# Performance work log

Hardware: AMD Instinct MI355X
Metric: run time of the kernel (lower is better)

Reference implementation:

```python
import jax, jax.numpy as jnp
import numpy as np

N_NODES = 10000
N_EDGES = 640000
D = 128


def setup_inputs() -> dict:
    key = jax.random.key(0)
    k1, k2, k3, k4 = jax.random.split(key, 4)
    X = jax.random.normal(k1, (N_NODES, D), dtype=jnp.float32)
    Y = jax.random.normal(k2, (N_EDGES, D), dtype=jnp.float32)
    # nn.Linear(in, out, bias=False): weight shape (out, in), y = Y @ W.T
    W = jax.random.normal(k3, (D, D), dtype=jnp.float32) * (1.0 / np.sqrt(D))
    edge_index = jax.random.randint(k4, (N_EDGES, 2), 0, N_NODES, dtype=jnp.int64)
    return {"X": X, "Y": Y, "W": W, "edge_index": edge_index}


def reference(X, Y, W, edge_index):
    # Edge transform: (E, d_in) @ (d_in, d_out) -> (E, d_out)
    Y_prime = jnp.einsum('ei,oi->eo', Y, W)
    # Scatter-add transformed edge features to source nodes
    src = edge_index[:, 0]
    agg = jax.ops.segment_sum(Y_prime, src, num_segments=X.shape[0])  # (N, d_out)
    # Residual + activation
    X_prime = jax.nn.relu(X + agg)
    return (X_prime, Y_prime)
```

## Files before the change

kernel.cpp:

```cpp
#include <hip/hip_runtime.h>

#define N_NODES 10000
#define N_EDGES 640000
#define DD 128
#define GATHER_BLOCKS (N_NODES / 4)
#define GEMM_BLOCKS   (N_EDGES / 128)

typedef __attribute__((ext_vector_type(8))) short short8;
typedef __attribute__((ext_vector_type(8))) float f32x8;
typedef __attribute__((ext_vector_type(4))) float f32x4;
typedef __attribute__((ext_vector_type(2))) float f32x2;

__device__ __forceinline__ unsigned pack_bf2(float lo, float hi) {
  return __builtin_amdgcn_perm(__float_as_uint(hi), __float_as_uint(lo), 0x07060302u);
}

__device__ __forceinline__ void stage_w(const float* __restrict__ W,
                                        short8* lwr) {
  const int tid = threadIdx.x;
#pragma unroll
  for (int t = 0; t < 8; ++t) {
    int s = t * 256 + tid;
    f32x8 v = *(const f32x8*)(W + (size_t)s * 8);
    short8 av;
    unsigned* au = (unsigned*)&av;
    au[0] = pack_bf2(v[0], v[1]);
    au[1] = pack_bf2(v[2], v[3]);
    au[2] = pack_bf2(v[4], v[5]);
    au[3] = pack_bf2(v[6], v[7]);
    int j = s >> 4;
    int c = s & 15;
    lwr[(j << 4) | (c ^ (j & 7))] = av;
  }
  __syncthreads();
}

__global__ __launch_bounds__(256) void k_zero(int* __restrict__ count) {
  const int i = blockIdx.x * 256 + threadIdx.x;
  if (i < N_NODES) count[i] = 0;
}

__global__ __launch_bounds__(256) void k_hist(const int* __restrict__ EI,
                                              int* __restrict__ count) {
  const int e = blockIdx.x * 256 + threadIdx.x;
  atomicAdd(&count[EI[2 * e]], 1);
}

__global__ __launch_bounds__(1024) void k_scan(const int* __restrict__ count,
                                               int* __restrict__ rowptr,
                                               int* __restrict__ cursor) {
  __shared__ int part[1024];
  const int tid = threadIdx.x;
  const int base = tid * 10;
  int local[10];
  int s = 0;
#pragma unroll
  for (int i = 0; i < 10; ++i) {
    const int idx = base + i;
    const int v = (idx < N_NODES) ? count[idx] : 0;
    local[i] = s;
    s += v;
  }
  part[tid] = s;
  __syncthreads();
  for (int off = 1; off < 1024; off <<= 1) {
    int v = 0;
    if (tid >= off) v = part[tid - off];
    __syncthreads();
    if (tid >= off) part[tid] += v;
    __syncthreads();
  }
  const int excl = (tid > 0) ? part[tid - 1] : 0;
#pragma unroll
  for (int i = 0; i < 10; ++i) {
    const int idx = base + i;
    if (idx < N_NODES) {
      const int r = excl + local[i];
      rowptr[idx] = r;
      cursor[idx] = r;
    }
  }
  if (tid == 1023) rowptr[N_NODES] = part[1023];
}

__global__ __launch_bounds__(256) void k_fill(const int* __restrict__ EI,
                                              int* __restrict__ cursor,
                                              int* __restrict__ col) {
  const int e = blockIdx.x * 256 + threadIdx.x;
  const int s = EI[2 * e];
  const int pos = atomicAdd(&cursor[s], 1);
  col[pos] = e;
}

__global__ __launch_bounds__(256, 2) void k_main(
    const float* __restrict__ Y,
    const float* __restrict__ W,
    const int* __restrict__ rowptr,
    const int* __restrict__ col,
    float* __restrict__ Yp,
    float* __restrict__ segY) {
  __shared__ short8 lwr[2048];

  if (blockIdx.x < GATHER_BLOCKS) {
    const int node = blockIdx.x * 4 + (threadIdx.x >> 6);
    const int lane = threadIdx.x & 63;
    const size_t co = 2 * lane;
    const int b  = rowptr[node];
    const int en = rowptr[node + 1];

    f32x2 acc = (f32x2){0.f, 0.f};
    int i = b;
    for (; i + 8 <= en; i += 8) {
      f32x2 v0 = *(const f32x2*)(Y + (size_t)col[i]     * DD + co);
      f32x2 v1 = *(const f32x2*)(Y + (size_t)col[i + 1] * DD + co);
      f32x2 v2 = *(const f32x2*)(Y + (size_t)col[i + 2] * DD + co);
      f32x2 v3 = *(const f32x2*)(Y + (size_t)col[i + 3] * DD + co);
      f32x2 v4 = *(const f32x2*)(Y + (size_t)col[i + 4] * DD + co);
      f32x2 v5 = *(const f32x2*)(Y + (size_t)col[i + 5] * DD + co);
      f32x2 v6 = *(const f32x2*)(Y + (size_t)col[i + 6] * DD + co);
      f32x2 v7 = *(const f32x2*)(Y + (size_t)col[i + 7] * DD + co);
      acc += v0; acc += v1; acc += v2; acc += v3;
      acc += v4; acc += v5; acc += v6; acc += v7;
    }
    for (; i < en; ++i) {
      acc += *(const f32x2*)(Y + (size_t)col[i] * DD + co);
    }
    *(f32x2*)(segY + (size_t)node * DD + co) = acc;
    return;
  }

  stage_w(W, lwr);
  const int wid  = threadIdx.x >> 6;
  const int lane = threadIdx.x & 63;
  const int l15  = lane & 15;
  const int lg   = lane >> 4;
  const int koff = lg * 8;
  const int ebase = (blockIdx.x - GATHER_BLOCKS) * 128 + wid * 32;

  short8 a[2][4];
#pragma unroll
  for (int mt = 0; mt < 2; ++mt) {
    const float* yr = Y + (size_t)(ebase + mt * 16 + l15) * DD;
#pragma unroll
    for (int kk = 0; kk < 4; ++kk) {
      f32x8 v = *(const f32x8*)(yr + kk * 32 + koff);
      short8 av;
      unsigned* au = (unsigned*)&av;
      au[0] = pack_bf2(v[0], v[1]);
      au[1] = pack_bf2(v[2], v[3]);
      au[2] = pack_bf2(v[4], v[5]);
      au[3] = pack_bf2(v[6], v[7]);
      a[mt][kk] = av;
    }
  }

  f32x4 acc[2][8];
#pragma unroll
  for (int mt = 0; mt < 2; ++mt)
#pragma unroll
    for (int nt = 0; nt < 8; ++nt)
      acc[mt][nt] = (f32x4){0.f, 0.f, 0.f, 0.f};

#pragma unroll
  for (int nt = 0; nt < 8; ++nt) {
    const int j = nt * 16 + l15;
#pragma unroll
    for (int kk = 0; kk < 4; ++kk) {
      const int kc = kk * 4 + lg;
      short8 b = lwr[(j << 4) | (kc ^ (j & 7))];
      acc[0][nt] = __builtin_amdgcn_mfma_f32_16x16x32_bf16(b, a[0][kk], acc[0][nt], 0, 0, 0);
      acc[1][nt] = __builtin_amdgcn_mfma_f32_16x16x32_bf16(b, a[1][kk], acc[1][nt], 0, 0, 0);
    }
  }

#pragma unroll
  for (int mt = 0; mt < 2; ++mt) {
    float* orow = Yp + (size_t)(ebase + mt * 16 + l15) * DD + lg * 4;
#pragma unroll
    for (int nt = 0; nt < 8; ++nt)
      __builtin_nontemporal_store(acc[mt][nt], (f32x4*)(orow + nt * 16));
  }
}

__global__ __launch_bounds__(256, 2) void k_small(
    const float* __restrict__ segY,
    const float* __restrict__ W,
    const float* __restrict__ X,
    float* __restrict__ Xp) {
  __shared__ short8 lwr[2048];
  stage_w(W, lwr);
  const int wid  = threadIdx.x >> 6;
  const int lane = threadIdx.x & 63;
  const int l15  = lane & 15;
  const int lg   = lane >> 4;
  const int koff = lg * 8;
  const int rbase = blockIdx.x * 128 + wid * 32;

  short8 a[2][4];
#pragma unroll
  for (int mt = 0; mt < 2; ++mt) {
    int row = rbase + mt * 16 + l15;
    if (row > N_NODES - 1) row = N_NODES - 1;
    const float* sr = segY + (size_t)row * DD + koff;
#pragma unroll
    for (int kk = 0; kk < 4; ++kk) {
      f32x8 v = *(const f32x8*)(sr + kk * 32);
      short8 av;
      unsigned* au = (unsigned*)&av;
      au[0] = pack_bf2(v[0], v[1]);
      au[1] = pack_bf2(v[2], v[3]);
      au[2] = pack_bf2(v[4], v[5]);
      au[3] = pack_bf2(v[6], v[7]);
      a[mt][kk] = av;
    }
  }

  f32x4 acc[2][8];
#pragma unroll
  for (int mt = 0; mt < 2; ++mt)
#pragma unroll
    for (int nt = 0; nt < 8; ++nt)
      acc[mt][nt] = (f32x4){0.f, 0.f, 0.f, 0.f};

#pragma unroll
  for (int nt = 0; nt < 8; ++nt) {
    const int j = nt * 16 + l15;
#pragma unroll
    for (int kk = 0; kk < 4; ++kk) {
      const int kc = kk * 4 + lg;
      short8 b = lwr[(j << 4) | (kc ^ (j & 7))];
      acc[0][nt] = __builtin_amdgcn_mfma_f32_16x16x32_bf16(b, a[0][kk], acc[0][nt], 0, 0, 0);
      acc[1][nt] = __builtin_amdgcn_mfma_f32_16x16x32_bf16(b, a[1][kk], acc[1][nt], 0, 0, 0);
    }
  }

#pragma unroll
  for (int mt = 0; mt < 2; ++mt) {
    const int row = rbase + mt * 16 + l15;
    if (row < N_NODES) {
      const float* xr   = X  + (size_t)row * DD + lg * 4;
      float*       orow = Xp + (size_t)row * DD + lg * 4;
#pragma unroll
      for (int nt = 0; nt < 8; ++nt) {
        f32x4 x = *(const f32x4*)(xr + nt * 16);
        f32x4 v = acc[mt][nt] + x;
        f32x4 r;
        r[0] = v[0] > 0.f ? v[0] : 0.f;
        r[1] = v[1] > 0.f ? v[1] : 0.f;
        r[2] = v[2] > 0.f ? v[2] : 0.f;
        r[3] = v[3] > 0.f ? v[3] : 0.f;
        *(f32x4*)(orow + nt * 16) = r;
      }
    }
  }
}

extern "C" void kernel_launch(void* const* d_in, const int* in_sizes, int n_in,
                              void* d_out, int out_size, void* d_ws, size_t ws_size,
                              hipStream_t stream) {
  const float* X  = (const float*)d_in[0];
  const float* Y  = (const float*)d_in[1];
  const float* W  = (const float*)d_in[2];
  const int*   EI = (const int*)d_in[3];

  float* Xp = (float*)d_out;
  float* Yp = Xp + (size_t)N_NODES * DD;

  int* w      = (int*)d_ws;
  int* count  = w;
  int* rowptr = w + 10000;
  int* cursor = w + 20001;
  int* col    = w + 30001;
  float* segY = (float*)(w + 670001 + 15);

  k_zero<<<(N_NODES + 255) / 256, 256, 0, stream>>>(count);
  k_hist<<<N_EDGES / 256, 256, 0, stream>>>(EI, count);
  k_scan<<<1, 1024, 0, stream>>>(count, rowptr, cursor);
  k_fill<<<N_EDGES / 256, 256, 0, stream>>>(EI, cursor, col);
  k_main<<<GATHER_BLOCKS + GEMM_BLOCKS, 256, 0, stream>>>(Y, W, rowptr, col, Yp, segY);
  k_small<<<(N_NODES + 127) / 128, 256, 0, stream>>>(segY, W, X, Xp);
}
```

Measured before the change: 313.6 us.

## Fuse edge GEMM and CSR-sorted segment gather into one kernel with atomics

Merges the separate gather and GEMM block roles into one kernel where each block handles 256 CSR-sorted edge slots. It runs the MFMA transform on the edges in sorted order, then sums the same Y rows per node within its slice and flushes partial sums with float atomics into a zeroed segY. The aim is to reuse Y rows that were just loaded, so they hit in cache, and to balance load by edge count instead of node degree. In exchange, segY must be zeroed up front, k_fill writes an extra nid array, atomic contention appears at slice boundaries, and the float summation order becomes nondeterministic.

Result: slower. 363.1 us (+15.8%).

```diff
diff --git a/kernel.cpp b/kernel.cpp
--- a/kernel.cpp
+++ b/kernel.cpp
@@ -3,8 +3,6 @@
 #define N_NODES 10000
 #define N_EDGES 640000
 #define DD 128
-#define GATHER_BLOCKS (N_NODES / 4)
-#define GEMM_BLOCKS   (N_EDGES / 128)
 
 typedef __attribute__((ext_vector_type(8))) short short8;
 typedef __attribute__((ext_vector_type(8))) float f32x8;
@@ -15,8 +13,8 @@
   return __builtin_amdgcn_perm(__float_as_uint(hi), __float_as_uint(lo), 0x07060302u);
 }
 
-__device__ __forceinline__ void stage_w(const float* __restrict__ W,
-                                        short8* lwr) {
+__device__ __forceinline__ void stage_w256(const float* __restrict__ W,
+                                           short8* lwr) {
   const int tid = threadIdx.x;
 #pragma unroll
   for (int t = 0; t < 8; ++t) {
@@ -35,9 +33,11 @@
   __syncthreads();
 }
 
-__global__ __launch_bounds__(256) void k_zero(int* __restrict__ count) {
+__global__ __launch_bounds__(256) void k_zero(int* __restrict__ count,
+                                              float* __restrict__ segY) {
   const int i = blockIdx.x * 256 + threadIdx.x;
   if (i < N_NODES) count[i] = 0;
+  if (i < N_NODES * DD) segY[i] = 0.f;
 }
 
 __global__ __launch_bounds__(256) void k_hist(const int* __restrict__ EI,
@@ -85,62 +85,38 @@
 
 __global__ __launch_bounds__(256) void k_fill(const int* __restrict__ EI,
                                               int* __restrict__ cursor,
-                                              int* __restrict__ col) {
+                                              int* __restrict__ col,
+                                              int* __restrict__ nid) {
   const int e = blockIdx.x * 256 + threadIdx.x;
   const int s = EI[2 * e];
   const int pos = atomicAdd(&cursor[s], 1);
   col[pos] = e;
-}
-
-__global__ __launch_bounds__(256, 2) void k_main(
+  nid[pos] = s;
+}
+
+__global__ __launch_bounds__(256, 2) void k_mega(
     const float* __restrict__ Y,
     const float* __restrict__ W,
-    const int* __restrict__ rowptr,
     const int* __restrict__ col,
+    const int* __restrict__ nid,
     float* __restrict__ Yp,
     float* __restrict__ segY) {
   __shared__ short8 lwr[2048];
-
-  if (blockIdx.x < GATHER_BLOCKS) {
-    const int node = blockIdx.x * 4 + (threadIdx.x >> 6);
-    const int lane = threadIdx.x & 63;
-    const size_t co = 2 * lane;
-    const int b  = rowptr[node];
-    const int en = rowptr[node + 1];
-
-    f32x2 acc = (f32x2){0.f, 0.f};
-    int i = b;
-    for (; i + 8 <= en; i += 8) {
-      f32x2 v0 = *(const f32x2*)(Y + (size_t)col[i]     * DD + co);
-      f32x2 v1 = *(const f32x2*)(Y + (size_t)col[i + 1] * DD + co);
-      f32x2 v2 = *(const f32x2*)(Y + (size_t)col[i + 2] * DD + co);
-      f32x2 v3 = *(const f32x2*)(Y + (size_t)col[i + 3] * DD + co);
-      f32x2 v4 = *(const f32x2*)(Y + (size_t)col[i + 4] * DD + co);
-      f32x2 v5 = *(const f32x2*)(Y + (size_t)col[i + 5] * DD + co);
-      f32x2 v6 = *(const f32x2*)(Y + (size_t)col[i + 6] * DD + co);
-      f32x2 v7 = *(const f32x2*)(Y + (size_t)col[i + 7] * DD + co);
-      acc += v0; acc += v1; acc += v2; acc += v3;
-      acc += v4; acc += v5; acc += v6; acc += v7;
-    }
-    for (; i < en; ++i) {
-      acc += *(const f32x2*)(Y + (size_t)col[i] * DD + co);
-    }
-    *(f32x2*)(segY + (size_t)node * DD + co) = acc;
-    return;
-  }
-
-  stage_w(W, lwr);
+  stage_w256(W, lwr);
   const int wid  = threadIdx.x >> 6;
   const int lane = threadIdx.x & 63;
   const int l15  = lane & 15;
   const int lg   = lane >> 4;
   const int koff = lg * 8;
-  const int ebase = (blockIdx.x - GATHER_BLOCKS) * 128 + wid * 32;
-
-  short8 a[2][4];
-#pragma unroll
-  for (int mt = 0; mt < 2; ++mt) {
-    const float* yr = Y + (size_t)(ebase + mt * 16 + l15) * DD;
+  const int base = blockIdx.x * 256;
+
+#pragma unroll 1
+  for (int it = 0; it < 4; ++it) {
+    const int p = base + it * 64 + wid * 16 + l15;
+    const int e = col[p];
+    const float* yr = Y + (size_t)e * DD;
+
+    short8 a[4];
 #pragma unroll
     for (int kk = 0; kk < 4; ++kk) {
       f32x8 v = *(const f32x8*)(yr + kk * 32 + koff);
@@ -150,36 +126,65 @@
       au[1] = pack_bf2(v[2], v[3]);
       au[2] = pack_bf2(v[4], v[5]);
       au[3] = pack_bf2(v[6], v[7]);
-      a[mt][kk] = av;
-    }
-  }
-
-  f32x4 acc[2][8];
-#pragma unroll
-  for (int mt = 0; mt < 2; ++mt)
+      a[kk] = av;
+    }
+
+    f32x4 acc[8];
 #pragma unroll
     for (int nt = 0; nt < 8; ++nt)
-      acc[mt][nt] = (f32x4){0.f, 0.f, 0.f, 0.f};
-
-#pragma unroll
-  for (int nt = 0; nt < 8; ++nt) {
-    const int j = nt * 16 + l15;
-#pragma unroll
-    for (int kk = 0; kk < 4; ++kk) {
-      const int kc = kk * 4 + lg;
-      short8 b = lwr[(j << 4) | (kc ^ (j & 7))];
-      acc[0][nt] = __builtin_amdgcn_mfma_f32_16x16x32_bf16(b, a[0][kk], acc[0][nt], 0, 0, 0);
-      acc[1][nt] = __builtin_amdgcn_mfma_f32_16x16x32_bf16(b, a[1][kk], acc[1][nt], 0, 0, 0);
-    }
-  }
-
-#pragma unroll
-  for (int mt = 0; mt < 2; ++mt) {
-    float* orow = Yp + (size_t)(ebase + mt * 16 + l15) * DD + lg * 4;
+      acc[nt] = (f32x4){0.f, 0.f, 0.f, 0.f};
+
+#pragma unroll
+    for (int nt = 0; nt < 8; ++nt) {
+      const int j = nt * 16 + l15;
+#pragma unroll
+      for (int kk = 0; kk < 4; ++kk) {
+        const int kc = kk * 4 + lg;
+        short8 b = lwr[(j << 4) | (kc ^ (j & 7))];
+        acc[nt] = __builtin_amdgcn_mfma_f32_16x16x32_bf16(b, a[kk], acc[nt], 0, 0, 0);
+      }
+    }
+
+    float* orow = Yp + (size_t)e * DD + lg * 4;
 #pragma unroll
     for (int nt = 0; nt < 8; ++nt)
-      __builtin_nontemporal_store(acc[mt][nt], (f32x4*)(orow + nt * 16));
-  }
+      __builtin_nontemporal_store(acc[nt], (f32x4*)(orow + nt * 16));
+  }
+
+  const int q0 = base + wid * 64;
+  const size_t co = 2 * (size_t)lane;
+  f32x2 acc2 = (f32x2){0.f, 0.f};
+  int cur = nid[q0];
+  int j = 0;
+#pragma unroll 1
+  while (j < 64) {
+    if (j + 8 <= 64 && nid[q0 + j + 7] == cur) {
+      const int p = q0 + j;
+      f32x2 v0 = *(const f32x2*)(Y + (size_t)col[p]     * DD + co);
+      f32x2 v1 = *(const f32x2*)(Y + (size_t)col[p + 1] * DD + co);
+      f32x2 v2 = *(const f32x2*)(Y + (size_t)col[p + 2] * DD + co);
+      f32x2 v3 = *(const f32x2*)(Y + (size_t)col[p + 3] * DD + co);
+      f32x2 v4 = *(const f32x2*)(Y + (size_t)col[p + 4] * DD + co);
+      f32x2 v5 = *(const f32x2*)(Y + (size_t)col[p + 5] * DD + co);
+      f32x2 v6 = *(const f32x2*)(Y + (size_t)col[p + 6] * DD + co);
+      f32x2 v7 = *(const f32x2*)(Y + (size_t)col[p + 7] * DD + co);
+      acc2 += v0; acc2 += v1; acc2 += v2; acc2 += v3;
+      acc2 += v4; acc2 += v5; acc2 += v6; acc2 += v7;
+      j += 8;
+    } else {
+      const int n = nid[q0 + j];
+      if (n != cur) {
+        unsafeAtomicAdd(&segY[(size_t)cur * DD + co],     acc2[0]);
+        unsafeAtomicAdd(&segY[(size_t)cur * DD + co + 1], acc2[1]);
+        acc2 = (f32x2){0.f, 0.f};
+        cur = n;
+      }
+      acc2 += *(const f32x2*)(Y + (size_t)col[q0 + j] * DD + co);
+      ++j;
+    }
+  }
+  unsafeAtomicAdd(&segY[(size_t)cur * DD + co],     acc2[0]);
+  unsafeAtomicAdd(&segY[(size_t)cur * DD + co + 1], acc2[1]);
 }
 
 __global__ __launch_bounds__(256, 2) void k_small(
@@ -188,7 +193,7 @@
     const float* __restrict__ X,
     float* __restrict__ Xp) {
   __shared__ short8 lwr[2048];
-  stage_w(W, lwr);
+  stage_w256(W, lwr);
   const int wid  = threadIdx.x >> 6;
   const int lane = threadIdx.x & 63;
   const int l15  = lane & 15;
@@ -271,12 +276,13 @@
   int* rowptr = w + 10000;
   int* cursor = w + 20001;
   int* col    = w + 30001;
-  float* segY = (float*)(w + 670001 + 15);
-
-  k_zero<<<(N_NODES + 255) / 256, 256, 0, stream>>>(count);
+  int* nid    = w + 670001;
+  float* segY = (float*)(w + 1310016);
+
+  k_zero<<<(N_NODES * DD + 255) / 256, 256, 0, stream>>>(count, segY);
   k_hist<<<N_EDGES / 256, 256, 0, stream>>>(EI, count);
   k_scan<<<1, 1024, 0, stream>>>(count, rowptr, cursor);
-  k_fill<<<N_EDGES / 256, 256, 0, stream>>>(EI, cursor, col);
-  k_main<<<GATHER_BLOCKS + GEMM_BLOCKS, 256, 0, stream>>>(Y, W, rowptr, col, Yp, segY);
+  k_fill<<<N_EDGES / 256, 256, 0, stream>>>(EI, cursor, col, nid);
+  k_mega<<<N_EDGES / 256, 256, 0, stream>>>(Y, W, col, nid, Yp, segY);
   k_small<<<(N_NODES + 127) / 128, 256, 0, stream>>>(segY, W, X, Xp);
 }
```
